# Kernel tuning notes

Hardware: AMD Instinct MI355X
Metric: run time of the kernel (lower is better)

The kernel has to match this reference:

```python
import jax, jax.numpy as jnp
import numpy as np

DEPTH = 4
CH = 3
SIG_CHANNELS = 3 + 9 + 27 + 81  # signatory.signature_channels(3, 4) = 120


def _tp(a, b):
    # flattened tensor (outer) product: (N, p) x (N, q) -> (N, p*q), row-major (signatory ordering)
    return (a[:, :, None] * b[:, None, :]).reshape(a.shape[0], -1)


def _signature(path):
    """Depth-4 path signature of path: (N, T, 3) -> (N, 120).

    Segment signature of a linear piece with increment dx is exp(dx):
    levels dx^{otimes k} / k!. Segments are combined with Chen's identity
    via a lax.scan over the time axis.
    """
    dx = path[:, 1:, :] - path[:, :-1, :]  # (N, T-1, 3)
    N, Tm1, _ = dx.shape
    dt = path.dtype
    # per-segment signature levels (flattened)
    s1 = dx                                                                # (N,T-1,3)
    s2 = (s1[..., :, None] * dx[..., None, :]).reshape(N, Tm1, 9) / 2.0   # dx^2/2!
    s3 = (s2[..., :, None] * dx[..., None, :]).reshape(N, Tm1, 27) / 3.0  # dx^3/3!
    s4 = (s3[..., :, None] * dx[..., None, :]).reshape(N, Tm1, 81) / 4.0  # dx^4/4!
    segs = (jnp.moveaxis(s1, 1, 0), jnp.moveaxis(s2, 1, 0),
            jnp.moveaxis(s3, 1, 0), jnp.moveaxis(s4, 1, 0))  # time-leading for scan

    init = (jnp.zeros((N, 3), dt), jnp.zeros((N, 9), dt),
            jnp.zeros((N, 27), dt), jnp.zeros((N, 81), dt))

    def chen_step(carry, seg):
        c1, c2, c3, c4 = carry
        g1, g2, g3, g4 = seg
        n1 = c1 + g1
        n2 = c2 + _tp(c1, g1) + g2
        n3 = c3 + _tp(c2, g1) + _tp(c1, g2) + g3
        n4 = c4 + _tp(c3, g1) + _tp(c2, g2) + _tp(c1, g3) + g4
        return (n1, n2, n3, n4), None

    (c1, c2, c3, c4), _ = jax.lax.scan(chen_step, init, segs)
    return jnp.concatenate([c1, c2, c3, c4], axis=1)  # (N, 120)


def setup_inputs() -> dict:
    key = jax.random.key(0)
    k1, k2, k3, k4, k5 = jax.random.split(key, 5)
    B, T, V, M = 64, 300, 17, 2
    inp = jax.random.normal(k1, (B, CH, T, V, M), dtype=jnp.float32)
    fan1 = 34 * SIG_CHANNELS  # 4080
    W1 = jax.random.uniform(k2, (512, fan1), jnp.float32, -1.0, 1.0) / np.sqrt(fan1)
    b1 = jax.random.uniform(k3, (512,), jnp.float32, -1.0, 1.0) / np.sqrt(fan1)
    W2 = jax.random.uniform(k4, (155, 512), jnp.float32, -1.0, 1.0) / np.sqrt(512)
    b2 = jax.random.uniform(k5, (155,), jnp.float32, -1.0, 1.0) / np.sqrt(512)
    return {"inp": inp, "W1": W1, "b1": b1, "W2": W2, "b2": b2}


def reference(inp, W1, b1, W2, b2):
    B, _, T, V, M = inp.shape
    # order matches the torch loop: for v in range(17): for m in range(2)
    paths = jnp.transpose(inp, (0, 3, 4, 2, 1)).reshape(B * V * M, T, CH)  # (B*34, T, 3)
    sig = _signature(paths).reshape(B, V * M * SIG_CHANNELS)  # (B, 4080)
    h = sig @ W1.T + b1  # dropout is identity in eval mode
    return h @ W2.T + b2  # (B, 155)
```

## Files before the change

### kernel.cpp

```cpp
#include <hip/hip_runtime.h>
#include <hip/hip_bf16.h>

#define B_SZ 64
#define T_PTS 300
#define N_SEG 299
#define VM 34
#define NPATH (B_SZ*VM)
#define SIGC 120
#define FAN1 4080
#define H1 512
#define NOUT 155
#define GSZ 16
#define CHUNK 19
#define TT 75

__device__ __forceinline__ void sig_append(float a1[3], float a2[9], float a3[27], float a4[81],
                                           float d0, float d1, float d2) {
  float B1[3] = {d0, d1, d2};
  float Hh[3] = {0.5f * d0, 0.5f * d1, 0.5f * d2};
  float Tt[3] = {(1.0f / 3.0f) * d0, (1.0f / 3.0f) * d1, (1.0f / 3.0f) * d2};
  float Qq[3] = {0.25f * d0, 0.25f * d1, 0.25f * d2};
  float B2[9], B3[27];
#pragma unroll
  for (int i = 0; i < 3; i++)
#pragma unroll
    for (int j = 0; j < 3; j++) B2[i * 3 + j] = B1[i] * Hh[j];
#pragma unroll
  for (int e = 0; e < 27; e++) B3[e] = B2[e / 3] * Tt[e % 3];

#pragma unroll
  for (int e = 0; e < 81; e++) {
    float v = a4[e];
    v = fmaf(B3[e / 3], Qq[e % 3], v);
    v = fmaf(a3[e / 3], B1[e % 3], v);
    v = fmaf(a2[e / 9], B2[e % 9], v);
    v = fmaf(a1[e / 27], B3[e % 27], v);
    a4[e] = v;
  }
#pragma unroll
  for (int e = 0; e < 27; e++) {
    float v = a3[e] + B3[e];
    v = fmaf(a2[e / 3], B1[e % 3], v);
    v = fmaf(a1[e / 9], B2[e % 9], v);
    a3[e] = v;
  }
#pragma unroll
  for (int e = 0; e < 9; e++) a2[e] = fmaf(a1[e / 3], B1[e % 3], a2[e] + B2[e]);
  a1[0] += d0; a1[1] += d1; a1[2] += d2;
}

__global__ __launch_bounds__(256) void transpose_kernel(const float* __restrict__ inp,
                                                        float* __restrict__ tp,
                                                        const float* __restrict__ b1,
                                                        float* __restrict__ h) {
  const int b = blockIdx.x;
  const int tile = blockIdx.y;
  const int t0 = tile * TT;
  const int tid = threadIdx.x;
  __shared__ float lds[3 * TT * VM];

  const float* src = inp + (size_t)b * 3 * T_PTS * VM;
  for (int idx = tid; idx < 3 * TT * VM; idx += 256) {
    const int c = idx / (TT * VM);
    const int rem = idx - c * (TT * VM);
    lds[idx] = src[(c * T_PTS + t0) * VM + rem];
  }
  __syncthreads();

  for (int idx = tid; idx < VM * TT * 3; idx += 256) {
    const int vm = idx / (TT * 3);
    const int i = idx - vm * (TT * 3);
    const int tt = i / 3;
    const int c = i - tt * 3;
    tp[((size_t)(b * VM + vm) * T_PTS + t0 + tt) * 3 + c] = lds[(c * TT + tt) * VM + vm];
  }

  if (tile == 0) {
    for (int j = tid; j < H1; j += 256) h[b * H1 + j] = b1[j];
  }
}

__global__ __launch_bounds__(64)
__attribute__((amdgpu_waves_per_eu(1)))
void sig_kernel(const float* __restrict__ tp, float* __restrict__ sig) {
  const int lane = threadIdx.x & 63;
  const int g = lane >> 4;
  const int sub = lane & (GSZ - 1);
  const int p = blockIdx.x * 4 + g;
  const int t0 = sub * CHUNK;

  const float* bp = tp + (size_t)p * (T_PTS * 3) + t0 * 3;

  float a1[3], a2[9], a3[27], a4[81];
#pragma unroll
  for (int i = 0; i < 3; i++) a1[i] = 0.f;
#pragma unroll
  for (int i = 0; i < 9; i++) a2[i] = 0.f;
#pragma unroll
  for (int i = 0; i < 27; i++) a3[i] = 0.f;
#pragma unroll
  for (int i = 0; i < 81; i++) a4[i] = 0.f;

  float x0 = bp[0], x1 = bp[1], x2 = bp[2];
  for (int s = 0; s < CHUNK; s++) {
    const float y0 = bp[3 * s + 3];
    const float y1 = bp[3 * s + 4];
    const float y2 = bp[3 * s + 5];
    const bool valid = (t0 + s) < N_SEG;
    const float d0 = valid ? (y0 - x0) : 0.0f;
    const float d1 = valid ? (y1 - x1) : 0.0f;
    const float d2 = valid ? (y2 - x2) : 0.0f;
    sig_append(a1, a2, a3, a4, d0, d1, d2);
    x0 = y0; x1 = y1; x2 = y2;
  }

#pragma unroll
  for (int off = 1; off < GSZ; off <<= 1) {
    const float m = (sub + off < GSZ) ? 1.0f : 0.0f;
    float B1[3], B2[9], B3[27];
#pragma unroll
    for (int i = 0; i < 3; i++) B1[i] = m * __shfl_down(a1[i], off);
#pragma unroll
    for (int i = 0; i < 9; i++) B2[i] = m * __shfl_down(a2[i], off);
#pragma unroll
    for (int i = 0; i < 27; i++) B3[i] = m * __shfl_down(a3[i], off);

#pragma unroll
    for (int e = 0; e < 81; e++) {
      const float b4 = m * __shfl_down(a4[e], off);
      float v = a4[e] + b4;
      v = fmaf(a3[e / 3], B1[e % 3], v);
      v = fmaf(a2[e / 9], B2[e % 9], v);
      v = fmaf(a1[e / 27], B3[e % 27], v);
      a4[e] = v;
    }
#pragma unroll
    for (int e = 0; e < 27; e++) {
      float v = a3[e] + B3[e];
      v = fmaf(a2[e / 3], B1[e % 3], v);
      v = fmaf(a1[e / 9], B2[e % 9], v);
      a3[e] = v;
    }
#pragma unroll
    for (int e = 0; e < 9; e++) a2[e] = fmaf(a1[e / 3], B1[e % 3], a2[e] + B2[e]);
#pragma unroll
    for (int i = 0; i < 3; i++) a1[i] += B1[i];
  }

  if (sub == 0) {
    float* dst = sig + (size_t)p * SIGC;
#pragma unroll
    for (int i = 0; i < 3; i++) dst[i] = a1[i];
#pragma unroll
    for (int i = 0; i < 9; i++) dst[3 + i] = a2[i];
#pragma unroll
    for (int i = 0; i < 27; i++) dst[12 + i] = a3[i];
#pragma unroll
    for (int i = 0; i < 81; i++) dst[39 + i] = a4[i];
  }
}

__global__ __launch_bounds__(256) void gemm1_kernel(const float* __restrict__ S,
                                                    const float* __restrict__ W1,
                                                    float* __restrict__ h) {
  const int jt = blockIdx.x;
  const int ks = blockIdx.y;
  const int tid = threadIdx.x;
  __shared__ float Ss[64][103];
  __shared__ float Ws[16][103];
  const int k0 = ks * 510;
  const int r = tid >> 2;
  const int cq = tid & 3;
  float acc0 = 0.f, acc1 = 0.f, acc2 = 0.f, acc3 = 0.f;

  for (int kc = 0; kc < 5; kc++) {
    const int kb = k0 + kc * 102;
    __syncthreads();
    for (int idx = tid; idx < 64 * 102; idx += 256) {
      const int rr = idx / 102, kk = idx - rr * 102;
      Ss[rr][kk] = S[rr * FAN1 + kb + kk];
    }
    for (int idx = tid; idx < 16 * 102; idx += 256) {
      const int jj = idx / 102, kk = idx - jj * 102;
      Ws[jj][kk] = W1[(jt * 16 + jj) * FAN1 + kb + kk];
    }
    __syncthreads();
#pragma unroll 6
    for (int k = 0; k < 102; k++) {
      const float a = Ss[r][k];
      acc0 = fmaf(a, Ws[cq * 4 + 0][k], acc0);
      acc1 = fmaf(a, Ws[cq * 4 + 1][k], acc1);
      acc2 = fmaf(a, Ws[cq * 4 + 2][k], acc2);
      acc3 = fmaf(a, Ws[cq * 4 + 3][k], acc3);
    }
  }
  float* hp = h + r * H1 + jt * 16 + cq * 4;
  atomicAdd(hp + 0, acc0);
  atomicAdd(hp + 1, acc1);
  atomicAdd(hp + 2, acc2);
  atomicAdd(hp + 3, acc3);
}

__global__ __launch_bounds__(256) void gemm2_kernel(const float* __restrict__ h,
                                                    const float* __restrict__ W2,
                                                    const float* __restrict__ b2,
                                                    float* __restrict__ out) {
  const int b = blockIdx.x;
  const int jg = blockIdx.y;
  const int wave = threadIdx.x >> 6;
  const int lane = threadIdx.x & 63;
  const int j = jg * 4 + wave;
  if (j >= NOUT) return;
  const float* hb = h + b * H1;
  const float* w = W2 + j * H1;
  float acc = 0.f;
#pragma unroll
  for (int i = 0; i < 8; i++) {
    const int k = lane + i * 64;
    acc = fmaf(hb[k], w[k], acc);
  }
#pragma unroll
  for (int off = 32; off > 0; off >>= 1) acc += __shfl_down(acc, off, 64);
  if (lane == 0) out[b * NOUT + j] = acc + b2[j];
}

extern "C" void kernel_launch(void* const* d_in, const int* in_sizes, int n_in,
                              void* d_out, int out_size, void* d_ws, size_t ws_size,
                              hipStream_t stream) {
  const float* inp = (const float*)d_in[0];
  const float* W1  = (const float*)d_in[1];
  const float* b1  = (const float*)d_in[2];
  const float* W2  = (const float*)d_in[3];
  const float* b2  = (const float*)d_in[4];
  float* out = (float*)d_out;

  float* tpbuf = (float*)d_ws;
  float* sig   = tpbuf + (size_t)NPATH * T_PTS * 3;
  float* h     = sig + (size_t)NPATH * SIGC;

  transpose_kernel<<<dim3(B_SZ, 4), 256, 0, stream>>>(inp, tpbuf, b1, h);
  sig_kernel<<<NPATH / 4, 64, 0, stream>>>(tpbuf, sig);
  gemm1_kernel<<<dim3(32, 8), 256, 0, stream>>>(sig, W1, h);
  gemm2_kernel<<<dim3(64, 39), 256, 0, stream>>>(h, W2, b2, out);
}
```

Before: 138.9 us.

## Store signatures and hidden activations batch-minor; restructure both GEMMs around lane-per-batch

The signature kernel now writes its output transposed (feature-major, batch in the fastest dimension), and the hidden buffer is also kept transposed. GEMM1 drops its LDS tiling: each wave handles four output columns over a 510-wide K slice, with one batch row per lane, so signature loads are coalesced and W1 loads are wave-uniform scalar broadcasts. GEMM2 becomes one block per output column, splitting K across four waves and reducing through shared memory. This removes LDS staging and barriers in GEMM1 but does more global loads per FMA, and the transposed signature stores from sig_kernel are strided.

```diff
diff --git a/kernel.cpp b/kernel.cpp
--- a/kernel.cpp
+++ b/kernel.cpp
@@ -52,7 +52,7 @@
 __global__ __launch_bounds__(256) void transpose_kernel(const float* __restrict__ inp,
                                                         float* __restrict__ tp,
                                                         const float* __restrict__ b1,
-                                                        float* __restrict__ h) {
+                                                        float* __restrict__ ht) {
   const int b = blockIdx.x;
   const int tile = blockIdx.y;
   const int t0 = tile * TT;
@@ -76,13 +76,14 @@
   }
 
   if (tile == 0) {
-    for (int j = tid; j < H1; j += 256) h[b * H1 + j] = b1[j];
+    for (int idx = tid; idx < 8 * 64; idx += 256)
+      ht[(size_t)(8 * b) * 64 + idx] = b1[8 * b + (idx >> 6)];
   }
 }
 
 __global__ __launch_bounds__(64)
 __attribute__((amdgpu_waves_per_eu(1)))
-void sig_kernel(const float* __restrict__ tp, float* __restrict__ sig) {
+void sig_kernel(const float* __restrict__ tp, float* __restrict__ St) {
   const int lane = threadIdx.x & 63;
   const int g = lane >> 4;
   const int sub = lane & (GSZ - 1);
@@ -148,80 +149,71 @@
   }
 
   if (sub == 0) {
-    float* dst = sig + (size_t)p * SIGC;
-#pragma unroll
-    for (int i = 0; i < 3; i++) dst[i] = a1[i];
-#pragma unroll
-    for (int i = 0; i < 9; i++) dst[3 + i] = a2[i];
-#pragma unroll
-    for (int i = 0; i < 27; i++) dst[12 + i] = a3[i];
-#pragma unroll
-    for (int i = 0; i < 81; i++) dst[39 + i] = a4[i];
-  }
-}
-
-__global__ __launch_bounds__(256) void gemm1_kernel(const float* __restrict__ S,
+    const int b = p / VM;
+    const int vm = p - b * VM;
+    float* dst = St + (size_t)(vm * SIGC) * 64 + b;
+#pragma unroll
+    for (int i = 0; i < 3; i++) dst[(size_t)i * 64] = a1[i];
+#pragma unroll
+    for (int i = 0; i < 9; i++) dst[(size_t)(3 + i) * 64] = a2[i];
+#pragma unroll
+    for (int i = 0; i < 27; i++) dst[(size_t)(12 + i) * 64] = a3[i];
+#pragma unroll
+    for (int i = 0; i < 81; i++) dst[(size_t)(39 + i) * 64] = a4[i];
+  }
+}
+
+__global__ __launch_bounds__(256) void gemm1_kernel(const float* __restrict__ St,
                                                     const float* __restrict__ W1,
-                                                    float* __restrict__ h) {
-  const int jt = blockIdx.x;
-  const int ks = blockIdx.y;
-  const int tid = threadIdx.x;
-  __shared__ float Ss[64][103];
-  __shared__ float Ws[16][103];
-  const int k0 = ks * 510;
-  const int r = tid >> 2;
-  const int cq = tid & 3;
+                                                    float* __restrict__ ht) {
+  const int lane = threadIdx.x & 63;
+  int wave_id = (blockIdx.x * 256 + threadIdx.x) >> 6;
+  wave_id = __builtin_amdgcn_readfirstlane(wave_id);
+  const int ks = wave_id >> 7;
+  const int jg = wave_id & 127;
+
+  const float* stp = St + (size_t)(ks * 510) * 64 + lane;
+  const float* w1r = W1 + (size_t)(jg * 4) * FAN1 + ks * 510;
+
   float acc0 = 0.f, acc1 = 0.f, acc2 = 0.f, acc3 = 0.f;
-
-  for (int kc = 0; kc < 5; kc++) {
-    const int kb = k0 + kc * 102;
-    __syncthreads();
-    for (int idx = tid; idx < 64 * 102; idx += 256) {
-      const int rr = idx / 102, kk = idx - rr * 102;
-      Ss[rr][kk] = S[rr * FAN1 + kb + kk];
-    }
-    for (int idx = tid; idx < 16 * 102; idx += 256) {
-      const int jj = idx / 102, kk = idx - jj * 102;
-      Ws[jj][kk] = W1[(jt * 16 + jj) * FAN1 + kb + kk];
-    }
-    __syncthreads();
 #pragma unroll 6
-    for (int k = 0; k < 102; k++) {
-      const float a = Ss[r][k];
-      acc0 = fmaf(a, Ws[cq * 4 + 0][k], acc0);
-      acc1 = fmaf(a, Ws[cq * 4 + 1][k], acc1);
-      acc2 = fmaf(a, Ws[cq * 4 + 2][k], acc2);
-      acc3 = fmaf(a, Ws[cq * 4 + 3][k], acc3);
-    }
-  }
-  float* hp = h + r * H1 + jt * 16 + cq * 4;
-  atomicAdd(hp + 0, acc0);
-  atomicAdd(hp + 1, acc1);
-  atomicAdd(hp + 2, acc2);
-  atomicAdd(hp + 3, acc3);
-}
-
-__global__ __launch_bounds__(256) void gemm2_kernel(const float* __restrict__ h,
+  for (int k = 0; k < 510; k++) {
+    const float sv = stp[(size_t)k * 64];
+    acc0 = fmaf(w1r[k], sv, acc0);
+    acc1 = fmaf(w1r[FAN1 + k], sv, acc1);
+    acc2 = fmaf(w1r[2 * FAN1 + k], sv, acc2);
+    acc3 = fmaf(w1r[3 * FAN1 + k], sv, acc3);
+  }
+
+  float* hp = ht + (size_t)(jg * 4) * 64 + lane;
+  atomicAdd(hp + 0 * 64, acc0);
+  atomicAdd(hp + 1 * 64, acc1);
+  atomicAdd(hp + 2 * 64, acc2);
+  atomicAdd(hp + 3 * 64, acc3);
+}
+
+__global__ __launch_bounds__(256) void gemm2_kernel(const float* __restrict__ ht,
                                                     const float* __restrict__ W2,
                                                     const float* __restrict__ b2,
                                                     float* __restrict__ out) {
-  const int b = blockIdx.x;
-  const int jg = blockIdx.y;
-  const int wave = threadIdx.x >> 6;
+  const int j = blockIdx.x;
   const int lane = threadIdx.x & 63;
-  const int j = jg * 4 + wave;
-  if (j >= NOUT) return;
-  const float* hb = h + b * H1;
-  const float* w = W2 + j * H1;
+  int w = threadIdx.x >> 6;
+  w = __builtin_amdgcn_readfirstlane(w);
+  __shared__ float red[4][64];
+
+  const float* htp = ht + (size_t)(w * 128) * 64 + lane;
+  const float* w2r = W2 + (size_t)j * H1 + w * 128;
   float acc = 0.f;
-#pragma unroll
-  for (int i = 0; i < 8; i++) {
-    const int k = lane + i * 64;
-    acc = fmaf(hb[k], w[k], acc);
-  }
-#pragma unroll
-  for (int off = 32; off > 0; off >>= 1) acc += __shfl_down(acc, off, 64);
-  if (lane == 0) out[b * NOUT + j] = acc + b2[j];
+#pragma unroll 8
+  for (int k = 0; k < 128; k++) acc = fmaf(w2r[k], htp[(size_t)k * 64], acc);
+
+  red[w][lane] = acc;
+  __syncthreads();
+  if (threadIdx.x < 64) {
+    const float tot = red[0][lane] + red[1][lane] + red[2][lane] + red[3][lane];
+    out[(size_t)lane * NOUT + j] = tot + b2[j];
+  }
 }
 
 extern "C" void kernel_launch(void* const* d_in, const int* in_sizes, int n_in,
@@ -235,11 +227,11 @@
   float* out = (float*)d_out;
 
   float* tpbuf = (float*)d_ws;
-  float* sig   = tpbuf + (size_t)NPATH * T_PTS * 3;
-  float* h     = sig + (size_t)NPATH * SIGC;
-
-  transpose_kernel<<<dim3(B_SZ, 4), 256, 0, stream>>>(inp, tpbuf, b1, h);
-  sig_kernel<<<NPATH / 4, 64, 0, stream>>>(tpbuf, sig);
-  gemm1_kernel<<<dim3(32, 8), 256, 0, stream>>>(sig, W1, h);
-  gemm2_kernel<<<dim3(64, 39), 256, 0, stream>>>(h, W2, b2, out);
-}
+  float* St    = tpbuf + (size_t)NPATH * T_PTS * 3;
+  float* ht    = St + (size_t)FAN1 * 64;
+
+  transpose_kernel<<<dim3(B_SZ, 4), 256, 0, stream>>>(inp, tpbuf, b1, ht);
+  sig_kernel<<<NPATH / 4, 64, 0, stream>>>(tpbuf, St);
+  gemm1_kernel<<<256, 256, 0, stream>>>(St, W1, ht);
+  gemm2_kernel<<<NOUT, 256, 0, stream>>>(ht, W2, b2, out);
+}
```

Result: no change. 137.3 us (-1.1%).
